# Performance work log

Measured on AMD Instinct MI355X. Metric: run time of the kernel, lower is better.

Reference implementation:

```python
import jax, jax.numpy as jnp
import numpy as np

# TT factorization for fc1: 768 = 4*4*6*8 -> 3072 = 4*6*8*16, ranks (1,12,24,12,1)
# TT factorization for fc2: 3072 = 4*6*8*16 -> 768 = 4*4*6*8, ranks (1,12,24,12,1)
IN_F1, OUT_F1 = (4, 4, 6, 8), (4, 6, 8, 16)
IN_F2, OUT_F2 = (4, 6, 8, 16), (4, 4, 6, 8)
RANKS = (12, 24, 12)


def _core(key, shape, fan_in):
    return jax.random.normal(key, shape, dtype=jnp.float32) * (fan_in ** -0.5)


def make_tt_params(key, in_f, out_f, ranks):
    r = (1,) + tuple(ranks) + (1,)
    ks = jax.random.split(key, 5)
    # boundary cores squeeze the unit rank dims
    g1 = _core(ks[0], (in_f[0], out_f[0], r[1]), in_f[0])              # (i1,o1,r1)
    g2 = _core(ks[1], (r[1], in_f[1], out_f[1], r[2]), r[1] * in_f[1])  # (r1,i2,o2,r2)
    g3 = _core(ks[2], (r[2], in_f[2], out_f[2], r[3]), r[2] * in_f[2])  # (r2,i3,o3,r3)
    g4 = _core(ks[3], (r[3], in_f[3], out_f[3]), r[3] * in_f[3])        # (r3,i4,o4)
    b = jnp.zeros((int(np.prod(out_f)),), dtype=jnp.float32)
    return g1, g2, g3, g4, b


def tt_linear(x2d, g1, g2, g3, g4, bias, in_f):
    # x2d: (N, prod(in_f)) -> (N, prod(out_f))
    z = x2d.reshape((-1,) + tuple(in_f))                  # (b,i1,i2,i3,i4)
    z = jnp.einsum('bijkl,ipr->bjklpr', z, g1)            # (b,i2,i3,i4,o1,r1)
    z = jnp.einsum('bjklpr,rjqs->bklpqs', z, g2)          # (b,i3,i4,o1,o2,r2)
    z = jnp.einsum('bklpqs,sktu->blpqtu', z, g3)          # (b,i4,o1,o2,o3,r3)
    z = jnp.einsum('blpqtu,ulv->bpqtv', z, g4)            # (b,o1,o2,o3,o4)
    return z.reshape(z.shape[0], -1) + bias


def setup_inputs() -> dict:
    key = jax.random.key(0)
    kx, k1, k2 = jax.random.split(key, 3)
    x = jax.random.normal(kx, (2, 2048, 768), dtype=jnp.float32)
    g1a, g1b, g1c, g1d, b1 = make_tt_params(k1, IN_F1, OUT_F1, RANKS)
    g2a, g2b, g2c, g2d, b2 = make_tt_params(k2, IN_F2, OUT_F2, RANKS)
    return {"x": x, "g1a": g1a, "g1b": g1b, "g1c": g1c, "g1d": g1d, "b1": b1,
            "g2a": g2a, "g2b": g2b, "g2c": g2c, "g2d": g2d, "b2": b2}


def reference(x, g1a, g1b, g1c, g1d, b1, g2a, g2b, g2c, g2d, b2):
    B, S, D = x.shape
    h = tt_linear(x.reshape(-1, D), g1a, g1b, g1c, g1d, b1, IN_F1)  # (N, 3072)
    h = jax.nn.gelu(h, approximate=False)  # nn.GELU() default = exact erf
    # dropout: identity in eval mode
    y = tt_linear(h, g2a, g2b, g2c, g2d, b2, IN_F2)                 # (N, 768)
    return y.reshape(B, S, -1)
```

## Files before the change

### kernel.cpp

```cpp
#include <hip/hip_runtime.h>
#include <cstdint>
#include <cstddef>

typedef unsigned short u16;
typedef __attribute__((ext_vector_type(8))) __bf16 bf16x8;
typedef __attribute__((ext_vector_type(4))) float f32x4;

__device__ __forceinline__ u16 f2bf(float f) {
  unsigned u = __float_as_uint(f);
  u += 0x7FFFu + ((u >> 16) & 1u);
  return (u16)(u >> 16);
}

__device__ __forceinline__ float bf2f(u16 h) {
  return __uint_as_float(((unsigned)h) << 16);
}

__device__ __forceinline__ void async16(u16* lds, const u16* g) {
  __builtin_amdgcn_global_load_lds(
      (const __attribute__((address_space(1))) unsigned int*)g,
      (__attribute__((address_space(3))) unsigned int*)lds, 16, 0, 0);
}

__global__ __launch_bounds__(256)
void tt_pre(const float* __restrict__ gA1, const float* __restrict__ gB1,
            const float* __restrict__ gC1, const float* __restrict__ gD1,
            const float* __restrict__ gA2, const float* __restrict__ gB2,
            const float* __restrict__ gC2, const float* __restrict__ gD2,
            float* __restrict__ B12_1, float* __restrict__ B12_2,
            float* __restrict__ C1, float* __restrict__ C2) {
  int idx = blockIdx.x * 256 + threadIdx.x;
  if (idx < 9216) {
    int e = idx;
    int r2 = e % 24; int t = e / 24;
    int fo12 = t % 24, fi12 = t / 24;
    int i2 = fi12 % 4, i1 = fi12 / 4;
    int o2 = fo12 % 6, o1 = fo12 / 6;
    float s = 0.f;
#pragma unroll
    for (int r1 = 0; r1 < 12; ++r1)
      s += gA1[(i1 * 4 + o1) * 12 + r1] * gB1[((r1 * 4 + i2) * 6 + o2) * 24 + r2];
    B12_1[e] = s;
  } else if (idx < 18432) {
    int e = idx - 9216;
    int r2 = e % 24; int t = e / 24;
    int fo12 = t % 16, fi12 = t / 16;
    int i2 = fi12 % 6, i1 = fi12 / 6;
    int o2 = fo12 % 4, o1 = fo12 / 4;
    float s = 0.f;
#pragma unroll
    for (int r1 = 0; r1 < 12; ++r1)
      s += gA2[(i1 * 4 + o1) * 12 + r1] * gB2[((r1 * 6 + i2) * 4 + o2) * 24 + r2];
    B12_2[e] = s;
  } else if (idx < 165888) {
    int e = idx - 18432;
    int fi34 = e % 48; int t = e / 48;
    int fo34 = t % 128;
    int i3 = fi34 / 8, i4 = fi34 % 8;
    int o3 = fo34 / 16, o4 = fo34 % 16;
    int r2 = t / 128;
    float s = 0.f;
#pragma unroll
    for (int r3 = 0; r3 < 12; ++r3)
      s += gC1[((r2 * 6 + i3) * 8 + o3) * 12 + r3] * gD1[(r3 * 8 + i4) * 16 + o4];
    C1[e] = s;
  } else {
    int e = idx - 165888;
    int fi34 = e % 128; int t = e / 128;
    int fo34 = t % 48;
    int i3 = fi34 / 16, i4 = fi34 % 16;
    int o3 = fo34 / 8, o4 = fo34 % 8;
    int r2 = t / 48;
    float s = 0.f;
#pragma unroll
    for (int r3 = 0; r3 < 12; ++r3)
      s += gC2[((r2 * 8 + i3) * 6 + o3) * 12 + r3] * gD2[(r3 * 16 + i4) * 8 + o4];
    C2[e] = s;
  }
}

template <int FI12, int I34, int O12, int O34, int OG>
__global__ __launch_bounds__(256)
void tt_expand(const float* __restrict__ B12, const float* __restrict__ C34t,
               u16* __restrict__ Wt) {
  constexpr int R2 = 24;
  constexpr int Kin = FI12 * I34;
  constexpr int IC = Kin / 8;
  constexpr int I34C = I34 / 8;
  __shared__ float sB[FI12 * OG * 25];
  const int tid = threadIdx.x;
  const int by = blockIdx.y;
  for (int e = tid; e < FI12 * OG * R2; e += 256) {
    int r2 = e % R2; int t = e / R2;
    int f = t % OG; int fi12 = t / OG;
    sB[(fi12 * OG + f) * 25 + r2] = B12[(fi12 * O12 + by * OG + f) * R2 + r2];
  }
  __syncthreads();
  const int t = blockIdx.x * 256 + tid;
  const int fo34 = t / IC;
  const int ic = t % IC;
  const int fi12 = ic / I34C;
  const int fi34 = (ic % I34C) * 8;

  float acc[OG][8];
#pragma unroll
  for (int f = 0; f < OG; ++f)
#pragma unroll
    for (int k = 0; k < 8; ++k) acc[f][k] = 0.f;

  for (int r2 = 0; r2 < R2; ++r2) {
    const float4* cp = (const float4*)(C34t + ((size_t)(r2 * O34 + fo34) * I34 + fi34));
    float4 c0 = cp[0], c1 = cp[1];
    float c[8] = {c0.x, c0.y, c0.z, c0.w, c1.x, c1.y, c1.z, c1.w};
#pragma unroll
    for (int f = 0; f < OG; ++f) {
      float b = sB[(fi12 * OG + f) * 25 + r2];
#pragma unroll
      for (int k = 0; k < 8; ++k) acc[f][k] += b * c[k];
    }
  }
#pragma unroll
  for (int f = 0; f < OG; ++f) {
    int out = (by * OG + f) * O34 + fo34;
    u16 v[8];
#pragma unroll
    for (int k = 0; k < 8; ++k) v[k] = f2bf(acc[f][k]);
    *(uint4*)(Wt + (size_t)out * Kin + fi12 * I34 + fi34) = *(const uint4*)v;
  }
}

__global__ void cvt_f32_bf16(const float4* __restrict__ in, ushort4* __restrict__ out, int n4) {
  int i = blockIdx.x * 256 + threadIdx.x;
  if (i < n4) {
    float4 v = in[i];
    ushort4 o;
    o.x = f2bf(v.x); o.y = f2bf(v.y); o.z = f2bf(v.z); o.w = f2bf(v.w);
    out[i] = o;
  }
}

__global__ void reduceN8(const uint4* __restrict__ P, const float* __restrict__ bias,
                         float4* __restrict__ out4, int n8, int zstride8, int nz) {
  int i = blockIdx.x * 256 + threadIdx.x;
  if (i >= n8) return;
  int b0 = (i % 96) * 8;
  float a[8];
#pragma unroll
  for (int k = 0; k < 8; ++k) a[k] = bias[b0 + k];
  for (int s = 0; s < nz; ++s) {
    uint4 u = P[i + s * zstride8];
    const u16* up = (const u16*)&u;
#pragma unroll
    for (int k = 0; k < 8; ++k) a[k] += bf2f(up[k]);
  }
  out4[i * 2]     = (float4){a[0], a[1], a[2], a[3]};
  out4[i * 2 + 1] = (float4){a[4], a[5], a[6], a[7]};
}

template <bool GELU>
__global__ __launch_bounds__(256, 3)
void gemm_bt(const u16* __restrict__ A, const u16* __restrict__ Bt,
             const float* __restrict__ bias, u16* __restrict__ Out,
             int N, int K, int klen, size_t zstride) {
  __shared__ __align__(16) u16 As[128 * 32];
  __shared__ __align__(16) u16 Bs[128 * 32];
  const int tid = threadIdx.x;
  const int bm = blockIdx.x, bn = blockIdx.y;
  const int wave = tid >> 6, lane = tid & 63;
  const int wm = (wave & 1) * 64, wn = (wave >> 1) * 64;
  const int lr = lane & 15, lq = lane >> 4;

  const int srow = tid >> 2;
  const int scol = (tid & 3) * 8;
  const u16* Ag = A + (size_t)(bm * 128 + srow) * K + scol;
  const u16* Bg = Bt + (size_t)(bn * 128 + srow) * K + scol;
  u16* AsW = As + tid * 8;
  u16* BsW = Bs + tid * 8;

  f32x4 acc[4][4];
#pragma unroll
  for (int i = 0; i < 4; i++)
#pragma unroll
    for (int j = 0; j < 4; j++) acc[i][j] = (f32x4){0.f, 0.f, 0.f, 0.f};

  const int kbeg = blockIdx.z * klen;
  const int kend = kbeg + klen;
  for (int k0 = kbeg; k0 < kend; k0 += 32) {
    async16(AsW,        Ag + k0);
    async16(AsW + 2048, Ag + k0 + (size_t)64 * K);
    async16(BsW,        Bg + k0);
    async16(BsW + 2048, Bg + k0 + (size_t)64 * K);
    __syncthreads();
    bf16x8 af[4], bfr[4];
#pragma unroll
    for (int i = 0; i < 4; i++)
      af[i] = *(const bf16x8*)(As + (wm + i * 16 + lr) * 32 + lq * 8);
#pragma unroll
    for (int j = 0; j < 4; j++)
      bfr[j] = *(const bf16x8*)(Bs + (wn + j * 16 + lr) * 32 + lq * 8);
#pragma unroll
    for (int i = 0; i < 4; i++)
#pragma unroll
      for (int j = 0; j < 4; j++)
        acc[i][j] = __builtin_amdgcn_mfma_f32_16x16x32_bf16(af[i], bfr[j], acc[i][j], 0, 0, 0);
    __syncthreads();
  }

  u16* Op = Out + blockIdx.z * zstride;
  const int r0 = bm * 128 + wm + lq * 4;
  const int c0 = bn * 128 + wn + lr;
#pragma unroll
  for (int j = 0; j < 4; j++) {
    const int col = c0 + j * 16;
    const float bv = GELU ? bias[col] : 0.f;
#pragma unroll
    for (int i = 0; i < 4; i++) {
      const int row = r0 + i * 16;
#pragma unroll
      for (int r = 0; r < 4; r++) {
        float v = acc[i][j][r];
        if (GELU) {
          v += bv;
          v = 0.5f * v * (1.f + erff(v * 0.70710678118654752f));
        }
        Op[(size_t)(row + r) * N + col] = f2bf(v);
      }
    }
  }
}

extern "C" void kernel_launch(void* const* d_in, const int* in_sizes, int n_in,
                              void* d_out, int out_size, void* d_ws, size_t ws_size,
                              hipStream_t stream) {
  const float* x   = (const float*)d_in[0];
  const float* g1a = (const float*)d_in[1];
  const float* g1b = (const float*)d_in[2];
  const float* g1c = (const float*)d_in[3];
  const float* g1d = (const float*)d_in[4];
  const float* b1  = (const float*)d_in[5];
  const float* g2a = (const float*)d_in[6];
  const float* g2b = (const float*)d_in[7];
  const float* g2c = (const float*)d_in[8];
  const float* g2d = (const float*)d_in[9];
  const float* b2  = (const float*)d_in[10];
  float* out = (float*)d_out;

  char* ws = (char*)d_ws;
  u16* xb   = (u16*)(ws + 0);
  u16* W1t  = (u16*)(ws + 6291456);
  u16* W2t  = (u16*)(ws + 11010048);
  u16* h    = (u16*)(ws + 15728640);
  u16* Part = (u16*)(ws + 40894464);
  float* B12_1 = (float*)(ws + 40894464);
  float* B12_2 = (float*)(ws + 40894464 + 36864);
  float* C1    = (float*)(ws + 40894464 + 73728);
  float* C2    = (float*)(ws + 40894464 + 663552);

  cvt_f32_bf16<<<3072, 256, 0, stream>>>((const float4*)x, (ushort4*)xb, 786432);

  tt_pre<<<1224, 256, 0, stream>>>(g1a, g1b, g1c, g1d, g2a, g2b, g2c, g2d,
                                   B12_1, B12_2, C1, C2);

  tt_expand<16, 48, 24, 128, 4><<<dim3(48, 6), 256, 0, stream>>>(B12_1, C1, W1t);
  tt_expand<24, 128, 16, 48, 4><<<dim3(72, 4), 256, 0, stream>>>(B12_2, C2, W2t);

  gemm_bt<true><<<dim3(32, 24, 1), 256, 0, stream>>>(xb, W1t, b1, h, 3072, 768, 768, 0);
  gemm_bt<false><<<dim3(32, 6, 4), 256, 0, stream>>>(h, W2t, nullptr, Part,
                                                     768, 3072, 768, 3145728);
  reduceN8<<<1536, 256, 0, stream>>>((const uint4*)Part, b2,
                                     (float4*)out, 393216, 393216, 4);
}
```

Baseline: 183.0 us.

## Double-buffer GEMM LDS tiles and merge input conversion into TT precompute kernel

The GEMM main loop now uses two LDS buffers and issues the async global-to-LDS loads for the next K tile before running MFMA on the current one. This is meant to hide load latency behind compute. The cvt and tt_pre kernels are merged into one launch to save a launch. The epilogue is reordered to preload the bias values and write row-major. Doubling LDS per block to 32KB may lower occupancy under the launch bound of 3 blocks. The loop also assumes nIter is even, which holds for the current sizes (24 iterations).

```diff
diff --git a/kernel.cpp b/kernel.cpp
--- a/kernel.cpp
+++ b/kernel.cpp
@@ -23,13 +23,24 @@
 }
 
 __global__ __launch_bounds__(256)
-void tt_pre(const float* __restrict__ gA1, const float* __restrict__ gB1,
-            const float* __restrict__ gC1, const float* __restrict__ gD1,
-            const float* __restrict__ gA2, const float* __restrict__ gB2,
-            const float* __restrict__ gC2, const float* __restrict__ gD2,
-            float* __restrict__ B12_1, float* __restrict__ B12_2,
-            float* __restrict__ C1, float* __restrict__ C2) {
-  int idx = blockIdx.x * 256 + threadIdx.x;
+void prep(const float4* __restrict__ x4, ushort4* __restrict__ xb4,
+          const float* __restrict__ gA1, const float* __restrict__ gB1,
+          const float* __restrict__ gC1, const float* __restrict__ gD1,
+          const float* __restrict__ gA2, const float* __restrict__ gB2,
+          const float* __restrict__ gC2, const float* __restrict__ gD2,
+          float* __restrict__ B12_1, float* __restrict__ B12_2,
+          float* __restrict__ C1, float* __restrict__ C2) {
+  const int b = blockIdx.x;
+  const int tid = threadIdx.x;
+  if (b < 3072) {
+    int i = b * 256 + tid;
+    float4 v = x4[i];
+    ushort4 o;
+    o.x = f2bf(v.x); o.y = f2bf(v.y); o.z = f2bf(v.z); o.w = f2bf(v.w);
+    xb4[i] = o;
+    return;
+  }
+  int idx = (b - 3072) * 256 + tid;
   if (idx < 9216) {
     int e = idx;
     int r2 = e % 24; int t = e / 24;
@@ -114,9 +125,9 @@
     float c[8] = {c0.x, c0.y, c0.z, c0.w, c1.x, c1.y, c1.z, c1.w};
 #pragma unroll
     for (int f = 0; f < OG; ++f) {
-      float b = sB[(fi12 * OG + f) * 25 + r2];
-#pragma unroll
-      for (int k = 0; k < 8; ++k) acc[f][k] += b * c[k];
+      float bb = sB[(fi12 * OG + f) * 25 + r2];
+#pragma unroll
+      for (int k = 0; k < 8; ++k) acc[f][k] += bb * c[k];
     }
   }
 #pragma unroll
@@ -126,16 +137,6 @@
 #pragma unroll
     for (int k = 0; k < 8; ++k) v[k] = f2bf(acc[f][k]);
     *(uint4*)(Wt + (size_t)out * Kin + fi12 * I34 + fi34) = *(const uint4*)v;
-  }
-}
-
-__global__ void cvt_f32_bf16(const float4* __restrict__ in, ushort4* __restrict__ out, int n4) {
-  int i = blockIdx.x * 256 + threadIdx.x;
-  if (i < n4) {
-    float4 v = in[i];
-    ushort4 o;
-    o.x = f2bf(v.x); o.y = f2bf(v.y); o.z = f2bf(v.z); o.w = f2bf(v.w);
-    out[i] = o;
   }
 }
 
@@ -162,8 +163,8 @@
 void gemm_bt(const u16* __restrict__ A, const u16* __restrict__ Bt,
              const float* __restrict__ bias, u16* __restrict__ Out,
              int N, int K, int klen, size_t zstride) {
-  __shared__ __align__(16) u16 As[128 * 32];
-  __shared__ __align__(16) u16 Bs[128 * 32];
+  __shared__ __align__(16) u16 As[2][128 * 32];
+  __shared__ __align__(16) u16 Bs[2][128 * 32];
   const int tid = threadIdx.x;
   const int bm = blockIdx.x, bn = blockIdx.y;
   const int wave = tid >> 6, lane = tid & 63;
@@ -174,8 +175,8 @@
   const int scol = (tid & 3) * 8;
   const u16* Ag = A + (size_t)(bm * 128 + srow) * K + scol;
   const u16* Bg = Bt + (size_t)(bn * 128 + srow) * K + scol;
-  u16* AsW = As + tid * 8;
-  u16* BsW = Bs + tid * 8;
+  u16* AsW = &As[0][0] + tid * 8;
+  u16* BsW = &Bs[0][0] + tid * 8;
 
   f32x4 acc[4][4];
 #pragma unroll
@@ -184,46 +185,60 @@
     for (int j = 0; j < 4; j++) acc[i][j] = (f32x4){0.f, 0.f, 0.f, 0.f};
 
   const int kbeg = blockIdx.z * klen;
-  const int kend = kbeg + klen;
-  for (int k0 = kbeg; k0 < kend; k0 += 32) {
-    async16(AsW,        Ag + k0);
-    async16(AsW + 2048, Ag + k0 + (size_t)64 * K);
-    async16(BsW,        Bg + k0);
-    async16(BsW + 2048, Bg + k0 + (size_t)64 * K);
-    __syncthreads();
+  const int nIter = klen >> 5;
+
+  auto stage = [&](int buf, int k0) {
+    async16(AsW + buf * 4096,        Ag + k0);
+    async16(AsW + buf * 4096 + 2048, Ag + k0 + (size_t)64 * K);
+    async16(BsW + buf * 4096,        Bg + k0);
+    async16(BsW + buf * 4096 + 2048, Bg + k0 + (size_t)64 * K);
+  };
+  auto compute = [&](int buf) {
     bf16x8 af[4], bfr[4];
 #pragma unroll
     for (int i = 0; i < 4; i++)
-      af[i] = *(const bf16x8*)(As + (wm + i * 16 + lr) * 32 + lq * 8);
+      af[i] = *(const bf16x8*)(&As[buf][0] + (wm + i * 16 + lr) * 32 + lq * 8);
 #pragma unroll
     for (int j = 0; j < 4; j++)
-      bfr[j] = *(const bf16x8*)(Bs + (wn + j * 16 + lr) * 32 + lq * 8);
+      bfr[j] = *(const bf16x8*)(&Bs[buf][0] + (wn + j * 16 + lr) * 32 + lq * 8);
 #pragma unroll
     for (int i = 0; i < 4; i++)
 #pragma unroll
       for (int j = 0; j < 4; j++)
         acc[i][j] = __builtin_amdgcn_mfma_f32_16x16x32_bf16(af[i], bfr[j], acc[i][j], 0, 0, 0);
+  };
+
+  stage(0, kbeg);
+  for (int it = 0; it < nIter; it += 2) {
     __syncthreads();
+    if (it + 1 < nIter) stage(1, kbeg + (it + 1) * 32);
+    compute(0);
+    __syncthreads();
+    if (it + 2 < nIter) stage(0, kbeg + (it + 2) * 32);
+    compute(1);
   }
 
   u16* Op = Out + blockIdx.z * zstride;
   const int r0 = bm * 128 + wm + lq * 4;
   const int c0 = bn * 128 + wn + lr;
-#pragma unroll
-  for (int j = 0; j < 4; j++) {
-    const int col = c0 + j * 16;
-    const float bv = GELU ? bias[col] : 0.f;
-#pragma unroll
-    for (int i = 0; i < 4; i++) {
-      const int row = r0 + i * 16;
-#pragma unroll
-      for (int r = 0; r < 4; r++) {
+  float bv[4];
+  if (GELU) {
+#pragma unroll
+    for (int j = 0; j < 4; j++) bv[j] = bias[c0 + j * 16];
+  }
+#pragma unroll
+  for (int i = 0; i < 4; i++) {
+#pragma unroll
+    for (int r = 0; r < 4; r++) {
+      const size_t rowoff = (size_t)(r0 + i * 16 + r) * N;
+#pragma unroll
+      for (int j = 0; j < 4; j++) {
         float v = acc[i][j][r];
         if (GELU) {
-          v += bv;
+          v += bv[j];
           v = 0.5f * v * (1.f + erff(v * 0.70710678118654752f));
         }
-        Op[(size_t)(row + r) * N + col] = f2bf(v);
+        Op[rowoff + c0 + j * 16] = f2bf(v);
       }
     }
   }
@@ -256,10 +271,9 @@
   float* C1    = (float*)(ws + 40894464 + 73728);
   float* C2    = (float*)(ws + 40894464 + 663552);
 
-  cvt_f32_bf16<<<3072, 256, 0, stream>>>((const float4*)x, (ushort4*)xb, 786432);
-
-  tt_pre<<<1224, 256, 0, stream>>>(g1a, g1b, g1c, g1d, g2a, g2b, g2c, g2d,
-                                   B12_1, B12_2, C1, C2);
+  prep<<<4296, 256, 0, stream>>>((const float4*)x, (ushort4*)xb,
+                                 g1a, g1b, g1c, g1d, g2a, g2b, g2c, g2d,
+                                 B12_1, B12_2, C1, C2);
 
   tt_expand<16, 48, 24, 128, 4><<<dim3(48, 6), 256, 0, stream>>>(B12_1, C1, W1t);
   tt_expand<24, 128, 16, 48, 4><<<dim3(72, 4), 256, 0, stream>>>(B12_2, C2, W2t);
```

Measured after the change: 181.2 us. No clear change (-1.0%).
